# Optimization experiments

Measured on AMD Instinct MI355X. Metric: run time of the kernel, lower is better.

## Reference

```python
import jax, jax.numpy as jnp
import numpy as np

B, T, D_MODEL, N_HEAD = 2, 2048, 1024, 16
HEAD_DIM = D_MODEL // N_HEAD


def setup_inputs() -> dict:
    key = jax.random.key(0)
    ks = jax.random.split(key, 4)
    s = 0.02
    return {
        "x": jax.random.normal(ks[0], (B, T, D_MODEL), dtype=jnp.float32),
        "freqs_cis": jnp.zeros((T, HEAD_DIM // 2), dtype=jnp.float32),  # unused under ALiBi
        "Wq": jax.random.normal(ks[1], (D_MODEL, D_MODEL), dtype=jnp.float32) * s,
        "bq": jnp.zeros((D_MODEL,), dtype=jnp.float32),
        "Wkv": jax.random.normal(ks[2], (2 * D_MODEL, D_MODEL), dtype=jnp.float32) * s,
        "bkv": jnp.zeros((2 * D_MODEL,), dtype=jnp.float32),
        "Wo": jax.random.normal(ks[3], (D_MODEL, D_MODEL), dtype=jnp.float32) * s,
        "bo": jnp.zeros((D_MODEL,), dtype=jnp.float32),
    }


def reference(x, freqs_cis, Wq, bq, Wkv, bkv, Wo, bo):
    Bb, Tt, C = x.shape
    H, Dh = N_HEAD, HEAD_DIM
    # projections (torch Linear: x @ W^T + b)
    q = (x @ Wq.T + bq).reshape(Bb, Tt, H, Dh).transpose(0, 2, 1, 3)      # [B,H,T,Dh]
    kv = (x @ Wkv.T + bkv).reshape(Bb, Tt, 2, H, Dh).transpose(2, 0, 3, 1, 4)
    k, v = kv[0], kv[1]                                                    # [B,H,T,Dh]
    scores = jnp.einsum('bhqd,bhkd->bhqk', q, k) * (1.0 / np.sqrt(Dh))
    # ALiBi: linear slopes (1/H ... 1.0), bias = slope * (j - i)
    slopes = jnp.arange(1, H + 1, dtype=jnp.float32) / H                   # [H]
    pos = jnp.arange(Tt, dtype=jnp.float32)
    dist = pos[None, :] - pos[:, None]                                     # [T,T], j - i
    scores = scores + slopes[:, None, None] * dist[None]                   # broadcast over B
    # causal mask (upper triangle -> -inf)
    causal = pos[:, None] >= pos[None, :]                                  # [T,T] keep-mask
    scores = jnp.where(causal[None, None], scores, -jnp.inf)
    attn = jax.nn.softmax(scores, axis=-1)
    y = jnp.einsum('bhqk,bhkd->bhqd', attn, v)                             # [B,H,T,Dh]
    y = y.transpose(0, 2, 1, 3).reshape(Bb, Tt, C)
    return y @ Wo.T + bo
```

## Files before the change

### kernel.cpp

```cpp
#include <hip/hip_runtime.h>

typedef unsigned short u16;
typedef __bf16 bf16x8 __attribute__((ext_vector_type(8)));
typedef unsigned short u16x8 __attribute__((ext_vector_type(8)));
typedef float f32x4 __attribute__((ext_vector_type(4)));

#define GP 72
#define KEY(r) ((((r) ^ ((r) >> 3)) & 7) << 3)
#define VKEY(d) ((((d) >> 3) & 7) << 3)

static __device__ __forceinline__ u16 f2b(float f) {
  union { float f; unsigned u; } x; x.f = f;
  unsigned r = x.u + 0x7FFFu + ((x.u >> 16) & 1u);
  return (u16)(r >> 16);
}

static __device__ __forceinline__ bf16x8 ld_frag(const u16* p) {
  union { u16x8 s; bf16x8 b; } u;
  u.s = *reinterpret_cast<const u16x8*>(p);
  return u.b;
}

__global__ __launch_bounds__(256) void cvt_f32_bf16(const float* __restrict__ in,
                                                    u16* __restrict__ out, int n4) {
  int i = blockIdx.x * 256 + threadIdx.x;
  if (i >= n4) return;
  float4 v = reinterpret_cast<const float4*>(in)[i];
  ushort4 o;
  o.x = f2b(v.x); o.y = f2b(v.y); o.z = f2b(v.z); o.w = f2b(v.w);
  reinterpret_cast<ushort4*>(out)[i] = o;
}

__global__ __launch_bounds__(256) void gemm_bt2(
    const u16* __restrict__ A, const u16* __restrict__ Bt,
    const float* __restrict__ bias, void* __restrict__ outp,
    int M, int N, int K, float scale, int out_bf16) {
  __shared__ alignas(16) u16 As[128 * 64];
  __shared__ alignas(16) u16 Bs[64 * 64];
  const int tid = threadIdx.x, wid = tid >> 6, lane = tid & 63;
  const int wr = wid >> 1, wc = wid & 1;
  const int row0 = blockIdx.x * 128, col0 = blockIdx.y * 64;
  const int lr = lane >> 3;
  const int lc = (lane & 7) * 8;
  const int frow = lane & 15, fk = (lane >> 4) * 8;
  f32x4 acc[4][2] = {};

  for (int k0 = 0; k0 < K; k0 += 64) {
    __syncthreads();
#pragma unroll
    for (int t = 0; t < 4; ++t) {
      const int r = wid * 32 + t * 8 + lr;
      __builtin_amdgcn_global_load_lds(
          (const __attribute__((address_space(1))) unsigned int*)(
              A + (size_t)(row0 + r) * K + k0 + (lc ^ KEY(r))),
          (__attribute__((address_space(3))) unsigned int*)(As + (wid * 32 + t * 8) * 64),
          16, 0, 0);
    }
#pragma unroll
    for (int t = 0; t < 2; ++t) {
      const int r = wid * 16 + t * 8 + lr;
      __builtin_amdgcn_global_load_lds(
          (const __attribute__((address_space(1))) unsigned int*)(
              Bt + (size_t)(col0 + r) * K + k0 + (lc ^ KEY(r))),
          (__attribute__((address_space(3))) unsigned int*)(Bs + (wid * 16 + t * 8) * 64),
          16, 0, 0);
    }
    __syncthreads();
#pragma unroll
    for (int ks = 0; ks < 2; ++ks) {
      bf16x8 a[4], b[2];
#pragma unroll
      for (int m = 0; m < 4; ++m) {
        const int r = wr * 64 + m * 16 + frow;
        a[m] = ld_frag(&As[r * 64 + ((ks * 32 + fk) ^ KEY(r))]);
      }
#pragma unroll
      for (int n = 0; n < 2; ++n) {
        const int r = wc * 32 + n * 16 + frow;
        b[n] = ld_frag(&Bs[r * 64 + ((ks * 32 + fk) ^ KEY(r))]);
      }
#pragma unroll
      for (int m = 0; m < 4; ++m)
#pragma unroll
        for (int n = 0; n < 2; ++n)
          acc[m][n] = __builtin_amdgcn_mfma_f32_16x16x32_bf16(a[m], b[n], acc[m][n], 0, 0, 0);
    }
  }
  const int colL = lane & 15, rb = (lane >> 4) * 4;
#pragma unroll
  for (int n = 0; n < 2; ++n) {
    const int gc = col0 + wc * 32 + n * 16 + colL;
    const float bv = bias[gc];
#pragma unroll
    for (int m = 0; m < 4; ++m)
#pragma unroll
      for (int r = 0; r < 4; ++r) {
        const int gr = row0 + wr * 64 + m * 16 + rb + r;
        const float v = (acc[m][n][r] + bv) * scale;
        if (out_bf16) reinterpret_cast<u16*>(outp)[(size_t)gr * N + gc] = f2b(v);
        else reinterpret_cast<float*>(outp)[(size_t)gr * N + gc] = v;
      }
  }
}

__global__ __launch_bounds__(256) void attn_kernel(
    const u16* __restrict__ qb,
    const u16* __restrict__ kvb,
    u16* __restrict__ yb,
    int T) {
  const int C = 1024;
  const int bh = blockIdx.x;
  const int qt = gridDim.y - 1 - blockIdx.y;
  const int b = bh >> 4, h = bh & 15;
  const float slope = (float)(h + 1) * 0.0625f;
  const int tid = threadIdx.x, wid = tid >> 6, lane = tid & 63;
  const int qBase = qt * 64;

  __shared__ alignas(16) u16 Ks[64 * GP];
  __shared__ alignas(16) u16 Vt[64 * GP];
  __shared__ alignas(16) u16 Ps[4][16 * GP];

  const int frow = lane & 15, fk = (lane >> 4) * 8;
  const int col = lane & 15, rb = (lane >> 4) * 4;

  const int q_row = qBase + wid * 16 + frow;
  const u16* qp = qb + (size_t)(b * T + q_row) * C + h * 64;
  const bf16x8 aq0 = ld_frag(qp + fk);
  const bf16x8 aq1 = ld_frag(qp + 32 + fk);

  float mrow[4] = {-1e30f, -1e30f, -1e30f, -1e30f};
  float lrow[4] = {0.f, 0.f, 0.f, 0.f};
  f32x4 accO[4] = {};

  const int sr = tid >> 3;
  const int sc = (tid & 7) * 8;

  for (int kt = 0; kt <= qt; ++kt) {
    const int kBase = kt * 64;
    __syncthreads();
    {
      const size_t g0 = (size_t)(b * T + kBase + sr) * 2048 + h * 64 + sc;
      const size_t g1 = (size_t)(b * T + kBase + sr + 32) * 2048 + h * 64 + sc;
      *reinterpret_cast<int4*>(&Ks[sr * GP + sc]) = *reinterpret_cast<const int4*>(&kvb[g0]);
      *reinterpret_cast<int4*>(&Ks[(sr + 32) * GP + sc]) = *reinterpret_cast<const int4*>(&kvb[g1]);
      int4 v0 = *reinterpret_cast<const int4*>(&kvb[g0 + 1024]);
      int4 v1 = *reinterpret_cast<const int4*>(&kvb[g1 + 1024]);
      const u16* p0 = reinterpret_cast<const u16*>(&v0);
      const u16* p1 = reinterpret_cast<const u16*>(&v1);
      const int kx = VKEY(sc);
#pragma unroll
      for (int j = 0; j < 8; ++j) {
        const int d = sc + j;
        Vt[d * GP + (sr ^ kx)] = p0[j];
        Vt[d * GP + ((sr + 32) ^ kx)] = p1[j];
      }
    }
    __syncthreads();

    f32x4 accS[4] = {};
#pragma unroll
    for (int n = 0; n < 4; ++n) {
      bf16x8 bk0 = ld_frag(&Ks[(n * 16 + frow) * GP + fk]);
      accS[n] = __builtin_amdgcn_mfma_f32_16x16x32_bf16(aq0, bk0, accS[n], 0, 0, 0);
      bf16x8 bk1 = ld_frag(&Ks[(n * 16 + frow) * GP + 32 + fk]);
      accS[n] = __builtin_amdgcn_mfma_f32_16x16x32_bf16(aq1, bk1, accS[n], 0, 0, 0);
    }

#pragma unroll
    for (int r = 0; r < 4; ++r) {
      const int qg = qBase + wid * 16 + rb + r;
      float s[4];
      float tmax = -1e30f;
#pragma unroll
      for (int n = 0; n < 4; ++n) {
        const int kg = kBase + n * 16 + col;
        float v = accS[n][r] + slope * (float)(kg - qg);
        if (kg > qg) v = -1e30f;
        s[n] = v;
        tmax = fmaxf(tmax, v);
      }
      tmax = fmaxf(tmax, __shfl_xor(tmax, 1));
      tmax = fmaxf(tmax, __shfl_xor(tmax, 2));
      tmax = fmaxf(tmax, __shfl_xor(tmax, 4));
      tmax = fmaxf(tmax, __shfl_xor(tmax, 8));
      const float newm = fmaxf(mrow[r], tmax);
      const float corr = __expf(mrow[r] - newm);
      mrow[r] = newm;
      float psum = 0.f;
#pragma unroll
      for (int n = 0; n < 4; ++n) {
        const float p = __expf(s[n] - newm);
        psum += p;
        Ps[wid][(rb + r) * GP + n * 16 + col] = f2b(p);
      }
      psum += __shfl_xor(psum, 1);
      psum += __shfl_xor(psum, 2);
      psum += __shfl_xor(psum, 4);
      psum += __shfl_xor(psum, 8);
      lrow[r] = lrow[r] * corr + psum;
#pragma unroll
      for (int n = 0; n < 4; ++n) accO[n][r] *= corr;
    }

#pragma unroll
    for (int ks = 0; ks < 2; ++ks) {
      bf16x8 ap = ld_frag(&Ps[wid][frow * GP + ks * 32 + fk]);
#pragma unroll
      for (int n = 0; n < 4; ++n) {
        const int d = n * 16 + frow;
        bf16x8 bv = ld_frag(&Vt[d * GP + ((ks * 32 + fk) ^ VKEY(d))]);
        accO[n] = __builtin_amdgcn_mfma_f32_16x16x32_bf16(ap, bv, accO[n], 0, 0, 0);
      }
    }
  }

#pragma unroll
  for (int r = 0; r < 4; ++r) {
    const float inv = 1.0f / lrow[r];
    const int qg = qBase + wid * 16 + rb + r;
    u16* yrow = yb + (size_t)(b * T + qg) * C + h * 64;
#pragma unroll
    for (int n = 0; n < 4; ++n) yrow[n * 16 + col] = f2b(accO[n][r] * inv);
  }
}

extern "C" void kernel_launch(void* const* d_in, const int* in_sizes, int n_in,
                              void* d_out, int out_size, void* d_ws, size_t ws_size,
                              hipStream_t stream) {
  const float* x   = (const float*)d_in[0];
  const float* Wq  = (const float*)d_in[2];
  const float* bq  = (const float*)d_in[3];
  const float* Wkv = (const float*)d_in[4];
  const float* bkv = (const float*)d_in[5];
  const float* Wo  = (const float*)d_in[6];
  const float* bo  = (const float*)d_in[7];
  float* out = (float*)d_out;

  const int B = 2, T = 2048, C = 1024;
  const int M = B * T;

  char* ws = (char*)d_ws;
  u16* xb   = (u16*)(ws + 0);
  u16* wqb  = (u16*)(ws + 8388608);
  u16* wkvb = (u16*)(ws + 10485760);
  u16* wob  = (u16*)(ws + 14680064);
  u16* qb   = (u16*)(ws + 16777216);
  u16* kvb  = (u16*)(ws + 25165824);
  u16* yb   = (u16*)(ws + 41943040);

  cvt_f32_bf16<<<(M * C / 4 + 255) / 256, 256, 0, stream>>>(x, xb, M * C / 4);
  cvt_f32_bf16<<<(C * C / 4 + 255) / 256, 256, 0, stream>>>(Wq, wqb, C * C / 4);
  cvt_f32_bf16<<<(2 * C * C / 4 + 255) / 256, 256, 0, stream>>>(Wkv, wkvb, 2 * C * C / 4);
  cvt_f32_bf16<<<(C * C / 4 + 255) / 256, 256, 0, stream>>>(Wo, wob, C * C / 4);

  gemm_bt2<<<dim3(M / 128, C / 64), 256, 0, stream>>>(xb, wqb, bq, qb, M, C, C, 0.125f, 1);
  gemm_bt2<<<dim3(M / 128, 2 * C / 64), 256, 0, stream>>>(xb, wkvb, bkv, kvb, M, 2 * C, C, 1.0f, 1);
  attn_kernel<<<dim3(B * 16, T / 64), 256, 0, stream>>>(qb, kvb, yb, T);
  gemm_bt2<<<dim3(M / 128, C / 64), 256, 0, stream>>>(yb, wob, bo, out, M, C, C, 1.0f, 0);
}
```

Baseline: 238.2 us.

## Split long causal attention rows across two blocks and fuse Q/KV projections

Attention for the upper 16 query tiles is split into two KV-range halves, each writing bf16 partial outputs plus max/sum into scratch (overlapping xb, no longer needed). A new combine kernel merges the halves, which balances the triangular causal workload across more blocks. The Q and KV projection GEMMs are merged into one launch with 128-wide N tiles, and the GEMM is templated so the output-type branch resolves at compile time. The partials are stored in bf16 before normalization, which adds some rounding error, and the combine step is an extra launch.

```diff
diff --git a/kernel.cpp b/kernel.cpp
--- a/kernel.cpp
+++ b/kernel.cpp
@@ -5,14 +5,18 @@
 typedef unsigned short u16x8 __attribute__((ext_vector_type(8)));
 typedef float f32x4 __attribute__((ext_vector_type(4)));
 
+#define KEY(r) ((((r) ^ ((r) >> 3)) & 7) << 3)
 #define GP 72
-#define KEY(r) ((((r) ^ ((r) >> 3)) & 7) << 3)
 #define VKEY(d) ((((d) >> 3) & 7) << 3)
 
 static __device__ __forceinline__ u16 f2b(float f) {
   union { float f; unsigned u; } x; x.f = f;
   unsigned r = x.u + 0x7FFFu + ((x.u >> 16) & 1u);
   return (u16)(r >> 16);
+}
+
+static __device__ __forceinline__ float b2f(u16 s) {
+  union { unsigned u; float f; } z; z.u = (unsigned)s << 16; return z.f;
 }
 
 static __device__ __forceinline__ bf16x8 ld_frag(const u16* p) {
@@ -31,19 +35,20 @@
   reinterpret_cast<ushort4*>(out)[i] = o;
 }
 
-__global__ __launch_bounds__(256) void gemm_bt2(
+template <bool OUT_BF16, int BN>
+static __device__ __forceinline__ void gemm_body(
     const u16* __restrict__ A, const u16* __restrict__ Bt,
     const float* __restrict__ bias, void* __restrict__ outp,
-    int M, int N, int K, float scale, int out_bf16) {
+    int N, int K, int row0, int col0, float scale) {
+  constexpr int NF = BN / 32;
   __shared__ alignas(16) u16 As[128 * 64];
-  __shared__ alignas(16) u16 Bs[64 * 64];
+  __shared__ alignas(16) u16 Bs[BN * 64];
   const int tid = threadIdx.x, wid = tid >> 6, lane = tid & 63;
   const int wr = wid >> 1, wc = wid & 1;
-  const int row0 = blockIdx.x * 128, col0 = blockIdx.y * 64;
   const int lr = lane >> 3;
   const int lc = (lane & 7) * 8;
   const int frow = lane & 15, fk = (lane >> 4) * 8;
-  f32x4 acc[4][2] = {};
+  f32x4 acc[4][NF] = {};
 
   for (int k0 = 0; k0 < K; k0 += 64) {
     __syncthreads();
@@ -57,39 +62,39 @@
           16, 0, 0);
     }
 #pragma unroll
-    for (int t = 0; t < 2; ++t) {
-      const int r = wid * 16 + t * 8 + lr;
+    for (int t = 0; t < NF; ++t) {
+      const int r = wid * (BN / 4) + t * 8 + lr;
       __builtin_amdgcn_global_load_lds(
           (const __attribute__((address_space(1))) unsigned int*)(
               Bt + (size_t)(col0 + r) * K + k0 + (lc ^ KEY(r))),
-          (__attribute__((address_space(3))) unsigned int*)(Bs + (wid * 16 + t * 8) * 64),
+          (__attribute__((address_space(3))) unsigned int*)(Bs + (wid * (BN / 4) + t * 8) * 64),
           16, 0, 0);
     }
     __syncthreads();
 #pragma unroll
     for (int ks = 0; ks < 2; ++ks) {
-      bf16x8 a[4], b[2];
+      bf16x8 a[4], b[NF];
 #pragma unroll
       for (int m = 0; m < 4; ++m) {
         const int r = wr * 64 + m * 16 + frow;
         a[m] = ld_frag(&As[r * 64 + ((ks * 32 + fk) ^ KEY(r))]);
       }
 #pragma unroll
-      for (int n = 0; n < 2; ++n) {
-        const int r = wc * 32 + n * 16 + frow;
+      for (int n = 0; n < NF; ++n) {
+        const int r = wc * (BN / 2) + n * 16 + frow;
         b[n] = ld_frag(&Bs[r * 64 + ((ks * 32 + fk) ^ KEY(r))]);
       }
 #pragma unroll
       for (int m = 0; m < 4; ++m)
 #pragma unroll
-        for (int n = 0; n < 2; ++n)
+        for (int n = 0; n < NF; ++n)
           acc[m][n] = __builtin_amdgcn_mfma_f32_16x16x32_bf16(a[m], b[n], acc[m][n], 0, 0, 0);
     }
   }
   const int colL = lane & 15, rb = (lane >> 4) * 4;
 #pragma unroll
-  for (int n = 0; n < 2; ++n) {
-    const int gc = col0 + wc * 32 + n * 16 + colL;
+  for (int n = 0; n < NF; ++n) {
+    const int gc = col0 + wc * (BN / 2) + n * 16 + colL;
     const float bv = bias[gc];
 #pragma unroll
     for (int m = 0; m < 4; ++m)
@@ -97,23 +102,55 @@
       for (int r = 0; r < 4; ++r) {
         const int gr = row0 + wr * 64 + m * 16 + rb + r;
         const float v = (acc[m][n][r] + bv) * scale;
-        if (out_bf16) reinterpret_cast<u16*>(outp)[(size_t)gr * N + gc] = f2b(v);
-        else reinterpret_cast<float*>(outp)[(size_t)gr * N + gc] = v;
-      }
-  }
-}
-
-__global__ __launch_bounds__(256) void attn_kernel(
+        if constexpr (OUT_BF16)
+          reinterpret_cast<u16*>(outp)[(size_t)gr * N + gc] = f2b(v);
+        else
+          reinterpret_cast<float*>(outp)[(size_t)gr * N + gc] = v;
+      }
+  }
+}
+
+__global__ __launch_bounds__(256) void gemm_qkv(
+    const u16* __restrict__ xb, const u16* __restrict__ wqb,
+    const u16* __restrict__ wkvb, const float* __restrict__ bq,
+    const float* __restrict__ bkv, u16* __restrict__ qb, u16* __restrict__ kvb) {
+  const int row0 = blockIdx.x * 128;
+  const int by = blockIdx.y;
+  const u16* Bt; const float* bias; u16* out; int N, col0; float scale;
+  if (by < 8) { Bt = wqb;  bias = bq;  out = qb;  N = 1024; col0 = by * 128;      scale = 0.125f; }
+  else        { Bt = wkvb; bias = bkv; out = kvb; N = 2048; col0 = (by - 8) * 128; scale = 1.0f; }
+  gemm_body<true, 128>(xb, Bt, bias, out, N, 1024, row0, col0, scale);
+}
+
+__global__ __launch_bounds__(256) void gemm_o(
+    const u16* __restrict__ yb, const u16* __restrict__ wob,
+    const float* __restrict__ bo, float* __restrict__ out) {
+  gemm_body<false, 64>(yb, wob, bo, out, 1024, 1024, blockIdx.x * 128, blockIdx.y * 64, 1.0f);
+}
+
+__global__ __launch_bounds__(256) void attn_split(
     const u16* __restrict__ qb,
     const u16* __restrict__ kvb,
     u16* __restrict__ yb,
+    char* __restrict__ part,
     int T) {
   const int C = 1024;
   const int bh = blockIdx.x;
-  const int qt = gridDim.y - 1 - blockIdx.y;
   const int b = bh >> 4, h = bh & 15;
   const float slope = (float)(h + 1) * 0.0625f;
   const int tid = threadIdx.x, wid = tid >> 6, lane = tid & 63;
+
+  const int y = blockIdx.y;
+  int qt, t0, t1, pidx; bool direct;
+  if (y < 32) {
+    qt = 31 - (y >> 1);
+    const int c = y & 1, nt = qt + 1, half = (nt + 1) >> 1;
+    t0 = c ? half : 0; t1 = c ? nt : half;
+    direct = false;
+    pidx = ((bh << 4) + (qt - 16)) * 2 + c;
+  } else {
+    qt = 47 - y; t0 = 0; t1 = qt + 1; direct = true; pidx = 0;
+  }
   const int qBase = qt * 64;
 
   __shared__ alignas(16) u16 Ks[64 * GP];
@@ -135,7 +172,7 @@
   const int sr = tid >> 3;
   const int sc = (tid & 7) * 8;
 
-  for (int kt = 0; kt <= qt; ++kt) {
+  for (int kt = t0; kt < t1; ++kt) {
     const int kBase = kt * 64;
     __syncthreads();
     {
@@ -214,14 +251,56 @@
     }
   }
 
-#pragma unroll
-  for (int r = 0; r < 4; ++r) {
-    const float inv = 1.0f / lrow[r];
-    const int qg = qBase + wid * 16 + rb + r;
-    u16* yrow = yb + (size_t)(b * T + qg) * C + h * 64;
-#pragma unroll
-    for (int n = 0; n < 4; ++n) yrow[n * 16 + col] = f2b(accO[n][r] * inv);
-  }
+  if (direct) {
+#pragma unroll
+    for (int r = 0; r < 4; ++r) {
+      const float inv = 1.0f / lrow[r];
+      const int qg = qBase + wid * 16 + rb + r;
+      u16* yrow = yb + (size_t)(b * T + qg) * C + h * 64;
+#pragma unroll
+      for (int n = 0; n < 4; ++n) yrow[n * 16 + col] = f2b(accO[n][r] * inv);
+    }
+  } else {
+    u16* Orec = (u16*)(part + (size_t)pidx * 8704);
+    float* mrec = (float*)(part + (size_t)pidx * 8704 + 8192);
+#pragma unroll
+    for (int r = 0; r < 4; ++r) {
+      const int row = wid * 16 + rb + r;
+#pragma unroll
+      for (int n = 0; n < 4; ++n)
+        Orec[row * 64 + n * 16 + col] = f2b(accO[n][r]);
+      if (col == 0) { mrec[row] = mrow[r]; mrec[64 + row] = lrow[r]; }
+    }
+  }
+}
+
+__global__ __launch_bounds__(256) void attn_combine(
+    const char* __restrict__ part, u16* __restrict__ yb, int T) {
+  const int C = 1024;
+  const int bh = blockIdx.x, b = bh >> 4, h = bh & 15;
+  const int qt = 16 + blockIdx.y;
+  const int tid = threadIdx.x;
+  const int row = tid >> 2;
+  const int d0 = (tid & 3) * 16;
+  const size_t base = (size_t)(((bh << 4) + (qt - 16)) * 2) * 8704;
+  const char* r0 = part + base;
+  const char* r1 = part + base + 8704;
+  const float m0 = ((const float*)(r0 + 8192))[row];
+  const float l0 = ((const float*)(r0 + 8192))[64 + row];
+  const float m1 = ((const float*)(r1 + 8192))[row];
+  const float l1 = ((const float*)(r1 + 8192))[64 + row];
+  const float M = fmaxf(m0, m1);
+  const float w0 = __expf(m0 - M), w1 = __expf(m1 - M);
+  const float inv = 1.0f / (l0 * w0 + l1 * w1);
+  const u16* o0 = (const u16*)r0 + row * 64 + d0;
+  const u16* o1 = (const u16*)r1 + row * 64 + d0;
+  alignas(16) u16 outv[16];
+#pragma unroll
+  for (int j = 0; j < 16; ++j)
+    outv[j] = f2b((b2f(o0[j]) * w0 + b2f(o1[j]) * w1) * inv);
+  u16* yrow = yb + (size_t)(b * T + qt * 64 + row) * C + h * 64 + d0;
+  *reinterpret_cast<int4*>(yrow) = *reinterpret_cast<const int4*>(outv);
+  *reinterpret_cast<int4*>(yrow + 8) = *reinterpret_cast<const int4*>(outv + 8);
 }
 
 extern "C" void kernel_launch(void* const* d_in, const int* in_sizes, int n_in,
@@ -247,14 +326,15 @@
   u16* qb   = (u16*)(ws + 16777216);
   u16* kvb  = (u16*)(ws + 25165824);
   u16* yb   = (u16*)(ws + 41943040);
+  char* part = ws;
 
   cvt_f32_bf16<<<(M * C / 4 + 255) / 256, 256, 0, stream>>>(x, xb, M * C / 4);
   cvt_f32_bf16<<<(C * C / 4 + 255) / 256, 256, 0, stream>>>(Wq, wqb, C * C / 4);
   cvt_f32_bf16<<<(2 * C * C / 4 + 255) / 256, 256, 0, stream>>>(Wkv, wkvb, 2 * C * C / 4);
   cvt_f32_bf16<<<(C * C / 4 + 255) / 256, 256, 0, stream>>>(Wo, wob, C * C / 4);
 
-  gemm_bt2<<<dim3(M / 128, C / 64), 256, 0, stream>>>(xb, wqb, bq, qb, M, C, C, 0.125f, 1);
-  gemm_bt2<<<dim3(M / 128, 2 * C / 64), 256, 0, stream>>>(xb, wkvb, bkv, kvb, M, 2 * C, C, 1.0f, 1);
-  attn_kernel<<<dim3(B * 16, T / 64), 256, 0, stream>>>(qb, kvb, yb, T);
-  gemm_bt2<<<dim3(M / 128, C / 64), 256, 0, stream>>>(yb, wob, bo, out, M, C, C, 1.0f, 0);
-}
+  gemm_qkv<<<dim3(M / 128, 8 + 16), 256, 0, stream>>>(xb, wqb, wkvb, bq, bkv, qb, kvb);
+  attn_split<<<dim3(B * 16, 48), 256, 0, stream>>>(qb, kvb, yb, part, T);
+  attn_combine<<<dim3(B * 16, 16), 256, 0, stream>>>(part, yb, T);
+  gemm_o<<<dim3(M / 128, C / 64), 256, 0, stream>>>(yb, wob, bo, out);
+}
```

Measured after the change: 243.2 us. 1.02x slower.
